# Performance work log

Measured on AMD Instinct MI355X. Metric: run time of the kernel, lower is better.

The kernel has to match this reference:

```python
import jax, jax.numpy as jnp
import numpy as np

N = 50000      # nodes
E = 800000     # edges (before self-loops)
F_IN = 128     # in_dim
H = 8          # heads
C = 16         # out_dim per head
NEG_SLOPE = 0.2
EPS = 1e-5


def setup_inputs() -> dict:
    key = jax.random.key(0)
    ks = jax.random.split(key, 8)
    x = jax.random.normal(ks[0], (N, F_IN), dtype=jnp.float32)
    edge_index = jax.random.randint(ks[1], (2, E), 0, N, dtype=jnp.int64)
    # GAT linear weight (xavier-ish scale), stored as [F_IN, H*C]
    W_gat = jax.random.normal(ks[2], (F_IN, H * C), dtype=jnp.float32) * 0.1
    att_src = jax.random.normal(ks[3], (H, C), dtype=jnp.float32) * 0.1
    att_dst = jax.random.normal(ks[4], (H, C), dtype=jnp.float32) * 0.1
    bias_gat = jnp.zeros((H * C,), dtype=jnp.float32)
    W_skip = jax.random.normal(ks[5], (F_IN, H * C), dtype=jnp.float32) * 0.1
    gamma = jnp.ones((H * C,), dtype=jnp.float32)
    beta = jnp.zeros((H * C,), dtype=jnp.float32)
    return {"x": x, "edge_index": edge_index, "W_gat": W_gat,
            "att_src": att_src, "att_dst": att_dst, "bias_gat": bias_gat,
            "W_skip": W_skip, "gamma": gamma, "beta": beta}


def reference(x, edge_index, W_gat, att_src, att_dst, bias_gat, W_skip, gamma, beta):
    # PyG GATConv default: add self-loops
    loop = jnp.arange(N, dtype=edge_index.dtype)
    src = jnp.concatenate([edge_index[0], loop])  # [E+N]
    dst = jnp.concatenate([edge_index[1], loop])  # [E+N]

    h = (x @ W_gat).reshape(N, H, C)              # [N,H,C]
    a_src = jnp.sum(h * att_src, axis=-1)          # [N,H]
    a_dst = jnp.sum(h * att_dst, axis=-1)          # [N,H]

    e = jax.nn.leaky_relu(a_src[src] + a_dst[dst], NEG_SLOPE)   # [E+N,H]
    # segment softmax over destination nodes
    e_max = jax.ops.segment_max(e, dst, num_segments=N)         # [N,H]
    e_exp = jnp.exp(e - e_max[dst])
    denom = jax.ops.segment_sum(e_exp, dst, num_segments=N)     # [N,H]
    alpha = e_exp / denom[dst]                                   # [E+N,H]

    msg = alpha[:, :, None] * h[src]                             # [E+N,H,C]
    gat_out = jax.ops.segment_sum(msg, dst, num_segments=N)     # [N,H,C]
    gat_out = gat_out.reshape(N, H * C) + bias_gat

    skip_out = x @ W_skip                                        # [N,H*C]
    z = gat_out + 0.1 * skip_out

    mu = jnp.mean(z, axis=-1, keepdims=True)
    var = jnp.mean((z - mu) ** 2, axis=-1, keepdims=True)
    z = (z - mu) * jax.lax.rsqrt(var + EPS) * gamma + beta
    return jax.nn.elu(z)  # dropout is identity in eval mode
```

## Files before the change

kernel.cpp:

```cpp
#include <hip/hip_runtime.h>
#include <hip/hip_bf16.h>

#define N_NODES 50000
#define N_EDGES 800000
#define F_IN    128
#define HC      128
#define NR      8
#define RSZ     6250
#define NCH     16
#define CHSZ    50000

typedef __attribute__((ext_vector_type(8))) short bf16x8;
typedef __attribute__((ext_vector_type(4))) float f32x4;

__device__ __forceinline__ float bf2f(unsigned int u16) {
    return __uint_as_float(u16 << 16);
}
__device__ __forceinline__ unsigned int f2bf(float f) {
    unsigned int u = __float_as_uint(f);
    return (u + 0x7fffu + ((u >> 16) & 1u)) >> 16;
}

__global__ __launch_bounds__(256) void k_hist(
    const int* __restrict__ dst,
    const float* __restrict__ Wg, const float* __restrict__ Ws,
    unsigned short* __restrict__ Bfrag, int* __restrict__ part)
{
    const int bid = blockIdx.x;
    const int tid = threadIdx.x;
    if (bid < 128) {
        __shared__ int hist[RSZ];
        const int r = bid & 7, c = bid >> 3;
        const int nb = r * RSZ;
        for (int i = tid; i < RSZ; i += 256) hist[i] = 0;
        __syncthreads();
        const int4* d4 = (const int4*)(dst + c * CHSZ);
        for (int i = tid; i < CHSZ / 4; i += 256) {
            const int4 v = d4[i];
            int b;
            b = v.x - nb; if ((unsigned)b < (unsigned)RSZ) atomicAdd(&hist[b], 1);
            b = v.y - nb; if ((unsigned)b < (unsigned)RSZ) atomicAdd(&hist[b], 1);
            b = v.z - nb; if ((unsigned)b < (unsigned)RSZ) atomicAdd(&hist[b], 1);
            b = v.w - nb; if ((unsigned)b < (unsigned)RSZ) atomicAdd(&hist[b], 1);
        }
        __syncthreads();
        for (int i = tid; i < RSZ; i += 256)
            part[(size_t)(nb + i) * NCH + c] = hist[i];
    } else {
        const int g = (bid - 128) * 256 + tid;
        if (g < 4096) {
            const int lane = g & 63;
            const int kq = (g >> 6) & 3;
            const int nt = g >> 8;
            const int cc = nt * 16 + (lane & 15);
            const int kbase = kq * 32 + (lane >> 4) * 8;
            const float* Wsel = (cc < 128) ? (Wg + cc) : (Ws + cc - 128);
            unsigned int pk[4];
#pragma unroll
            for (int p = 0; p < 4; p++) {
                const float v0 = Wsel[(size_t)(kbase + 2 * p) * HC];
                const float v1 = Wsel[(size_t)(kbase + 2 * p + 1) * HC];
                pk[p] = f2bf(v0) | (f2bf(v1) << 16);
            }
            *(uint4*)(Bfrag + (size_t)g * 8) = make_uint4(pk[0], pk[1], pk[2], pk[3]);
        }
    }
}

__global__ __launch_bounds__(256) void k_merge(int* __restrict__ part,
                                               int* __restrict__ counts)
{
    const int n = blockIdx.x * 256 + threadIdx.x;
    if (n >= N_NODES) return;
    int4* p = (int4*)(part + (size_t)n * NCH);
    int4 v0 = p[0], v1 = p[1], v2 = p[2], v3 = p[3];
    int vv[16] = {v0.x, v0.y, v0.z, v0.w, v1.x, v1.y, v1.z, v1.w,
                  v2.x, v2.y, v2.z, v2.w, v3.x, v3.y, v3.z, v3.w};
    int run = 0;
#pragma unroll
    for (int c = 0; c < 16; c++) { const int t = vv[c]; vv[c] = run; run += t; }
    counts[n] = run;
    p[0] = make_int4(vv[0], vv[1], vv[2], vv[3]);
    p[1] = make_int4(vv[4], vv[5], vv[6], vv[7]);
    p[2] = make_int4(vv[8], vv[9], vv[10], vv[11]);
    p[3] = make_int4(vv[12], vv[13], vv[14], vv[15]);
}

__global__ __launch_bounds__(256) void k_scanA(const int* __restrict__ counts,
                                               int* __restrict__ row_start,
                                               int* __restrict__ bsum) {
    __shared__ int s[256];
    const int tid = threadIdx.x;
    const int base = blockIdx.x * 1024 + tid * 4;
    int v[4]; int t = 0;
#pragma unroll
    for (int j = 0; j < 4; j++) {
        int idx = base + j;
        v[j] = (idx < N_NODES) ? (counts[idx] + 1) : 0;
        t += v[j];
    }
    s[tid] = t;
    __syncthreads();
    for (int off = 1; off < 256; off <<= 1) {
        int add = (tid >= off) ? s[tid - off] : 0;
        __syncthreads();
        s[tid] += add;
        __syncthreads();
    }
    int excl = s[tid] - t;
#pragma unroll
    for (int j = 0; j < 4; j++) {
        int idx = base + j;
        if (idx < N_NODES) row_start[idx] = excl;
        excl += v[j];
    }
    if (tid == 255) bsum[blockIdx.x] = s[255];
}

__global__ void k_scanB(int* bsum, int nb) {
    int tid = threadIdx.x;
    int v = (tid < nb) ? bsum[tid] : 0;
    int orig = v;
    for (int off = 1; off < 64; off <<= 1) {
        int y = __shfl_up(v, off);
        if (tid >= off) v += y;
    }
    if (tid < nb) bsum[tid] = v - orig;
}

__global__ void k_scanC(int* __restrict__ row_start, const int* __restrict__ bsum,
                        const int* __restrict__ counts, int* __restrict__ csr) {
    int i = blockIdx.x * 256 + threadIdx.x;
    if (i < N_NODES) {
        int rs = row_start[i] + bsum[i >> 10];
        row_start[i] = rs;
        csr[rs + counts[i]] = i;
    }
}

__global__ __launch_bounds__(256) void k_lf(
    const float* __restrict__ x,
    const unsigned short* __restrict__ Bfrag,
    const float* __restrict__ att_s,
    const float* __restrict__ att_d,
    const float* __restrict__ bias,
    unsigned short* __restrict__ h_bf, unsigned int* __restrict__ z0b,
    float* __restrict__ a_src, float* __restrict__ a_dst,
    const int* __restrict__ src, const int* __restrict__ dst,
    const int* __restrict__ row_start, const int* __restrict__ part,
    int* __restrict__ csr)
{
    __shared__ __align__(16) int smem[RSZ];
    const int bid = blockIdx.x;
    const int tid = threadIdx.x;
    int lin = -1, r = 0, c = 0;
    if (bid < 256) {
        const int g = bid >> 4, pos = bid & 15;
        if (pos < 8) { r = pos; c = g; }
        else lin = g * 8 + (pos - 8);
    } else {
        lin = 128 + (bid - 256);
    }

    if (lin < 0) {
        const int nb = r * RSZ;
        for (int b = tid; b < RSZ; b += 256)
            smem[b] = row_start[nb + b] + part[(size_t)(nb + b) * NCH + c];
        __syncthreads();
        const int4* d4 = (const int4*)(dst + c * CHSZ);
        const int4* s4 = (const int4*)(src + c * CHSZ);
        for (int i = tid; i < CHSZ / 4; i += 256) {
            const int4 dv = d4[i];
            const int4 sv = s4[i];
            int b;
            b = dv.x - nb; if ((unsigned)b < (unsigned)RSZ) csr[atomicAdd(&smem[b], 1)] = sv.x;
            b = dv.y - nb; if ((unsigned)b < (unsigned)RSZ) csr[atomicAdd(&smem[b], 1)] = sv.y;
            b = dv.z - nb; if ((unsigned)b < (unsigned)RSZ) csr[atomicAdd(&smem[b], 1)] = sv.z;
            b = dv.w - nb; if ((unsigned)b < (unsigned)RSZ) csr[atomicAdd(&smem[b], 1)] = sv.w;
        }
        return;
    }

    unsigned short* sA = (unsigned short*)smem;
    const int lane = tid & 63;
    const int w = tid >> 6;
    const int nbase = lin * 64;

#pragma unroll
    for (int it = 0; it < 4; it++) {
        const int p = it * 256 + tid;
        const int node = p >> 4;
        const int kg = p & 15;
        const int gn = nbase + node;
        float v[8];
        if (gn < N_NODES) {
            float4 u0 = *(const float4*)(x + (size_t)gn * F_IN + kg * 8);
            float4 u1 = *(const float4*)(x + (size_t)gn * F_IN + kg * 8 + 4);
            v[0] = u0.x; v[1] = u0.y; v[2] = u0.z; v[3] = u0.w;
            v[4] = u1.x; v[5] = u1.y; v[6] = u1.z; v[7] = u1.w;
        } else {
#pragma unroll
            for (int j = 0; j < 8; j++) v[j] = 0.f;
        }
        const int mt = node >> 4, lm = node & 15;
        const int kq = kg >> 2, quad = kg & 3;
        uint4 pk;
        pk.x = f2bf(v[0]) | (f2bf(v[1]) << 16);
        pk.y = f2bf(v[2]) | (f2bf(v[3]) << 16);
        pk.z = f2bf(v[4]) | (f2bf(v[5]) << 16);
        pk.w = f2bf(v[6]) | (f2bf(v[7]) << 16);
        *(uint4*)(sA + ((size_t)((mt * 4 + kq) * 64 + quad * 16 + lm)) * 8) = pk;
    }
    __syncthreads();

    const bf16x8* Bf = (const bf16x8*)Bfrag;
    f32x4 acc[4][4];
#pragma unroll
    for (int mt = 0; mt < 4; mt++)
#pragma unroll
        for (int nt = 0; nt < 4; nt++)
            acc[mt][nt] = (f32x4){0.f, 0.f, 0.f, 0.f};

#pragma unroll
    for (int kq = 0; kq < 4; kq++) {
        bf16x8 aF[4], bF[4];
#pragma unroll
        for (int nt = 0; nt < 4; nt++)
            bF[nt] = Bf[(size_t)(((w * 4 + nt) * 4 + kq) * 64 + lane)];
#pragma unroll
        for (int mt = 0; mt < 4; mt++)
            aF[mt] = *(const bf16x8*)(sA + ((size_t)((mt * 4 + kq) * 64 + lane)) * 8);
#pragma unroll
        for (int mt = 0; mt < 4; mt++)
#pragma unroll
            for (int nt = 0; nt < 4; nt++)
                acc[mt][nt] = __builtin_amdgcn_mfma_f32_16x16x32_bf16(
                    aF[mt], bF[nt], acc[mt][nt], 0, 0, 0);
    }

    const int row4 = (lane >> 4) * 4;
    const int cl = lane & 15;
#pragma unroll
    for (int mt = 0; mt < 4; mt++) {
#pragma unroll
        for (int nt = 0; nt < 4; nt++) {
            const int cc = w * 64 + nt * 16 + cl;
            f32x4 d = acc[mt][nt];
            if (cc < 128) {
                const float asv = att_s[cc];
                const float adv = att_d[cc];
                float ps[4], pd[4];
#pragma unroll
                for (int rr = 0; rr < 4; rr++) { ps[rr] = d[rr] * asv; pd[rr] = d[rr] * adv; }
#pragma unroll
                for (int m = 1; m <= 8; m <<= 1) {
#pragma unroll
                    for (int rr = 0; rr < 4; rr++) {
                        ps[rr] += __shfl_xor(ps[rr], m);
                        pd[rr] += __shfl_xor(pd[rr], m);
                    }
                }
                const int head = w * 4 + nt;
#pragma unroll
                for (int rr = 0; rr < 4; rr++) {
                    const int gn = nbase + mt * 16 + row4 + rr;
                    if (gn < N_NODES) {
                        h_bf[(size_t)gn * HC + cc] = (unsigned short)f2bf(d[rr]);
                        if (cl == 0) {
                            a_src[gn * 8 + head] = ps[rr];
                            a_dst[gn * 8 + head] = pd[rr];
                        }
                    }
                }
            } else {
                const int cz = cc - 128;
                const float bv = bias[cz];
#pragma unroll
                for (int rr = 0; rr < 4; rr++) {
                    const int gn = nbase + mt * 16 + row4 + rr;
                    const float val = 0.1f * d[rr] + bv;
                    const float oth = __shfl_xor(val, 1);
                    if ((cl & 1) == 0 && gn < N_NODES) {
                        z0b[(size_t)gn * 64 + (cz >> 1)] =
                            f2bf(val) | (f2bf(oth) << 16);
                    }
                }
            }
        }
    }
}

__global__ __launch_bounds__(256) void k_agg(
    const uint2* __restrict__ h2,
    const uint2* __restrict__ z0b,
    const float* __restrict__ a_src, const float* __restrict__ a_dst,
    const int* __restrict__ row_start, const int* __restrict__ counts,
    const int* __restrict__ csr,
    const float* __restrict__ gamma, const float* __restrict__ beta,
    float* __restrict__ out)
{
    const int tid = threadIdx.x;
    const int lane = tid & 63;
    const int l = lane & 31;
    const int n = blockIdx.x * 8 + ((tid >> 6) << 1) + (lane >> 5);
    const int head = l >> 2;

    const float adn = a_dst[n * 8 + head];
    const int rs = row_start[n];
    const int cnt = counts[n] + 1;

    float d_acc = 0.f, a0 = 0.f, a1 = 0.f, a2 = 0.f, a3 = 0.f;
    for (int i = 0; i < cnt; i += 4) {
        int s[4]; float ae[4], mk[4]; uint2 hp[4];
#pragma unroll
        for (int j = 0; j < 4; j++) {
            const int e = i + j;
            const int ec = (e < cnt) ? e : (cnt - 1);
            mk[j] = (e < cnt) ? 1.f : 0.f;
            s[j] = csr[rs + ec];
        }
#pragma unroll
        for (int j = 0; j < 4; j++) ae[j] = a_src[s[j] * 8 + head];
#pragma unroll
        for (int j = 0; j < 4; j++) hp[j] = h2[(size_t)s[j] * 32 + l];
#pragma unroll
        for (int j = 0; j < 4; j++) {
            float e = ae[j] + adn;
            e = (e > 0.f) ? e : 0.2f * e;
            const float wgt = __expf(e) * mk[j];
            d_acc += wgt;
            a0 += wgt * bf2f(hp[j].x & 0xffffu);
            a1 += wgt * bf2f(hp[j].x >> 16);
            a2 += wgt * bf2f(hp[j].y & 0xffffu);
            a3 += wgt * bf2f(hp[j].y >> 16);
        }
    }
    const float inv = 1.0f / d_acc;
    const uint2 zp = z0b[(size_t)n * 32 + l];
    float y0 = a0 * inv + bf2f(zp.x & 0xffffu);
    float y1 = a1 * inv + bf2f(zp.x >> 16);
    float y2 = a2 * inv + bf2f(zp.y & 0xffffu);
    float y3 = a3 * inv + bf2f(zp.y >> 16);

    float ss = y0 + y1 + y2 + y3;
#pragma unroll
    for (int off = 1; off < 32; off <<= 1) ss += __shfl_xor(ss, off);
    const float mu = ss * (1.0f / 128.0f);
    const float d0 = y0 - mu, d1 = y1 - mu, d2 = y2 - mu, d3 = y3 - mu;
    float vs = d0 * d0 + d1 * d1 + d2 * d2 + d3 * d3;
#pragma unroll
    for (int off = 1; off < 32; off <<= 1) vs += __shfl_xor(vs, off);
    const float rstd = rsqrtf(vs * (1.0f / 128.0f) + 1e-5f);

    const float4 gv = *(const float4*)(gamma + l * 4);
    const float4 bv = *(const float4*)(beta + l * 4);
    float o0 = d0 * rstd * gv.x + bv.x;
    float o1 = d1 * rstd * gv.y + bv.y;
    float o2 = d2 * rstd * gv.z + bv.z;
    float o3 = d3 * rstd * gv.w + bv.w;
    o0 = (o0 > 0.f) ? o0 : (__expf(o0) - 1.0f);
    o1 = (o1 > 0.f) ? o1 : (__expf(o1) - 1.0f);
    o2 = (o2 > 0.f) ? o2 : (__expf(o2) - 1.0f);
    o3 = (o3 > 0.f) ? o3 : (__expf(o3) - 1.0f);

    *(float4*)(out + (size_t)n * HC + l * 4) = make_float4(o0, o1, o2, o3);
}

extern "C" void kernel_launch(void* const* d_in, const int* in_sizes, int n_in,
                              void* d_out, int out_size, void* d_ws, size_t ws_size,
                              hipStream_t stream) {
    const float* x   = (const float*)d_in[0];
    const int*   ei  = (const int*)d_in[1];
    const float* Wg  = (const float*)d_in[2];
    const float* as_ = (const float*)d_in[3];
    const float* ad_ = (const float*)d_in[4];
    const float* bg  = (const float*)d_in[5];
    const float* Wsk = (const float*)d_in[6];
    const float* gm  = (const float*)d_in[7];
    const float* bt  = (const float*)d_in[8];
    float* out = (float*)d_out;

    char* wsb = (char*)d_ws;
    unsigned short* h_bf  = (unsigned short*)wsb;
    unsigned int*   z0b   = (unsigned int*)(wsb + 12800000);
    float*          a_src = (float*)(wsb + 25600000);
    float*          a_dst = (float*)(wsb + 27200000);
    unsigned short* Bfrag = (unsigned short*)(wsb + 28800000);
    int*   counts = (int*)(wsb + 28865536);
    int*   row_st = (int*)(wsb + 29065728);
    int*   bsum   = (int*)(wsb + 29265920);
    int*   csr    = (int*)(wsb + 29266944);
    int*   part   = (int*)(wsb + 32666944);

    const int* src = ei;
    const int* dst = ei + N_EDGES;

    k_hist <<<144, 256, 0, stream>>>(dst, Wg, Wsk, Bfrag, part);
    k_merge<<<196, 256, 0, stream>>>(part, counts);
    k_scanA<<<49, 256, 0, stream>>>(counts, row_st, bsum);
    k_scanB<<<1, 64, 0, stream>>>(bsum, 49);
    k_scanC<<<196, 256, 0, stream>>>(row_st, bsum, counts, csr);
    k_lf   <<<910, 256, 0, stream>>>(x, Bfrag, as_, ad_, bg, h_bf, z0b,
                                     a_src, a_dst, src, dst, row_st, part, csr);
    k_agg  <<<N_NODES / 8, 256, 0, stream>>>((const uint2*)h_bf, (const uint2*)z0b,
                                             a_src, a_dst, row_st, counts, csr,
                                             gm, bt, out);
}
```

Measured before the change: 213.2 us.

## Split histogram/scatter into more node ranges, fold merge into scan, widen agg unroll

Doubles the number of destination-node ranges (16 ranges of 3125), so the histogram and CSR-scatter phases run on 256 blocks instead of 128, each with a smaller shared-memory table. The per-node prefix merge kernel is folded into the first scan kernel, which removes one launch and one pass over the partial counts. The scatter blocks in the fused linear kernel are interleaved one in four with the GEMM blocks. The aggregation loop now gathers 8 edges per iteration instead of 4, giving more loads in flight at the cost of more registers. In exchange, every block still rereads each 50000-edge chunk of the destination (and, in the scatter, source) arrays, so twice as many blocks means twice as much of that redundant reading.

```diff
diff --git a/kernel.cpp b/kernel.cpp
--- a/kernel.cpp
+++ b/kernel.cpp
@@ -5,8 +5,8 @@
 #define N_EDGES 800000
 #define F_IN    128
 #define HC      128
-#define NR      8
-#define RSZ     6250
+#define NR      16
+#define RSZ     3125
 #define NCH     16
 #define CHSZ    50000
 
@@ -28,9 +28,9 @@
 {
     const int bid = blockIdx.x;
     const int tid = threadIdx.x;
-    if (bid < 128) {
+    if (bid < 256) {
         __shared__ int hist[RSZ];
-        const int r = bid & 7, c = bid >> 3;
+        const int r = bid & 15, c = bid >> 4;
         const int nb = r * RSZ;
         for (int i = tid; i < RSZ; i += 256) hist[i] = 0;
         __syncthreads();
@@ -47,7 +47,7 @@
         for (int i = tid; i < RSZ; i += 256)
             part[(size_t)(nb + i) * NCH + c] = hist[i];
     } else {
-        const int g = (bid - 128) * 256 + tid;
+        const int g = (bid - 256) * 256 + tid;
         if (g < 4096) {
             const int lane = g & 63;
             const int kq = (g >> 6) & 3;
@@ -67,36 +67,32 @@
     }
 }
 
-__global__ __launch_bounds__(256) void k_merge(int* __restrict__ part,
-                                               int* __restrict__ counts)
+__global__ __launch_bounds__(256) void k_scanA(
+    int* __restrict__ part, int* __restrict__ counts,
+    int* __restrict__ row_start, int* __restrict__ bsum)
 {
-    const int n = blockIdx.x * 256 + threadIdx.x;
-    if (n >= N_NODES) return;
-    int4* p = (int4*)(part + (size_t)n * NCH);
-    int4 v0 = p[0], v1 = p[1], v2 = p[2], v3 = p[3];
-    int vv[16] = {v0.x, v0.y, v0.z, v0.w, v1.x, v1.y, v1.z, v1.w,
-                  v2.x, v2.y, v2.z, v2.w, v3.x, v3.y, v3.z, v3.w};
-    int run = 0;
-#pragma unroll
-    for (int c = 0; c < 16; c++) { const int t = vv[c]; vv[c] = run; run += t; }
-    counts[n] = run;
-    p[0] = make_int4(vv[0], vv[1], vv[2], vv[3]);
-    p[1] = make_int4(vv[4], vv[5], vv[6], vv[7]);
-    p[2] = make_int4(vv[8], vv[9], vv[10], vv[11]);
-    p[3] = make_int4(vv[12], vv[13], vv[14], vv[15]);
-}
-
-__global__ __launch_bounds__(256) void k_scanA(const int* __restrict__ counts,
-                                               int* __restrict__ row_start,
-                                               int* __restrict__ bsum) {
     __shared__ int s[256];
     const int tid = threadIdx.x;
     const int base = blockIdx.x * 1024 + tid * 4;
     int v[4]; int t = 0;
 #pragma unroll
     for (int j = 0; j < 4; j++) {
-        int idx = base + j;
-        v[j] = (idx < N_NODES) ? (counts[idx] + 1) : 0;
+        const int idx = base + j;
+        if (idx < N_NODES) {
+            int4* p = (int4*)(part + (size_t)idx * NCH);
+            int4 a0 = p[0], a1 = p[1], a2 = p[2], a3 = p[3];
+            int vv[16] = {a0.x, a0.y, a0.z, a0.w, a1.x, a1.y, a1.z, a1.w,
+                          a2.x, a2.y, a2.z, a2.w, a3.x, a3.y, a3.z, a3.w};
+            int run = 0;
+#pragma unroll
+            for (int c = 0; c < 16; c++) { const int q = vv[c]; vv[c] = run; run += q; }
+            p[0] = make_int4(vv[0], vv[1], vv[2], vv[3]);
+            p[1] = make_int4(vv[4], vv[5], vv[6], vv[7]);
+            p[2] = make_int4(vv[8], vv[9], vv[10], vv[11]);
+            p[3] = make_int4(vv[12], vv[13], vv[14], vv[15]);
+            counts[idx] = run;
+            v[j] = run + 1;
+        } else v[j] = 0;
         t += v[j];
     }
     s[tid] = t;
@@ -110,7 +106,7 @@
     int excl = s[tid] - t;
 #pragma unroll
     for (int j = 0; j < 4; j++) {
-        int idx = base + j;
+        const int idx = base + j;
         if (idx < N_NODES) row_start[idx] = excl;
         excl += v[j];
     }
@@ -150,35 +146,34 @@
     const int* __restrict__ row_start, const int* __restrict__ part,
     int* __restrict__ csr)
 {
-    __shared__ __align__(16) int smem[RSZ];
+    __shared__ __align__(16) int smem[4096];
     const int bid = blockIdx.x;
     const int tid = threadIdx.x;
-    int lin = -1, r = 0, c = 0;
-    if (bid < 256) {
-        const int g = bid >> 4, pos = bid & 15;
-        if (pos < 8) { r = pos; c = g; }
-        else lin = g * 8 + (pos - 8);
+    int lin;
+    if (bid < 1024) {
+        if ((bid & 3) == 0) {
+            const int f = bid >> 2;
+            const int r = f & 15, c = f >> 4;
+            const int nb = r * RSZ;
+            for (int b = tid; b < RSZ; b += 256)
+                smem[b] = row_start[nb + b] + part[(size_t)(nb + b) * NCH + c];
+            __syncthreads();
+            const int4* d4 = (const int4*)(dst + c * CHSZ);
+            const int4* s4 = (const int4*)(src + c * CHSZ);
+            for (int i = tid; i < CHSZ / 4; i += 256) {
+                const int4 dv = d4[i];
+                const int4 sv = s4[i];
+                int b;
+                b = dv.x - nb; if ((unsigned)b < (unsigned)RSZ) csr[atomicAdd(&smem[b], 1)] = sv.x;
+                b = dv.y - nb; if ((unsigned)b < (unsigned)RSZ) csr[atomicAdd(&smem[b], 1)] = sv.y;
+                b = dv.z - nb; if ((unsigned)b < (unsigned)RSZ) csr[atomicAdd(&smem[b], 1)] = sv.z;
+                b = dv.w - nb; if ((unsigned)b < (unsigned)RSZ) csr[atomicAdd(&smem[b], 1)] = sv.w;
+            }
+            return;
+        }
+        lin = bid - (bid >> 2) - 1;
     } else {
-        lin = 128 + (bid - 256);
-    }
-
-    if (lin < 0) {
-        const int nb = r * RSZ;
-        for (int b = tid; b < RSZ; b += 256)
-            smem[b] = row_start[nb + b] + part[(size_t)(nb + b) * NCH + c];
-        __syncthreads();
-        const int4* d4 = (const int4*)(dst + c * CHSZ);
-        const int4* s4 = (const int4*)(src + c * CHSZ);
-        for (int i = tid; i < CHSZ / 4; i += 256) {
-            const int4 dv = d4[i];
-            const int4 sv = s4[i];
-            int b;
-            b = dv.x - nb; if ((unsigned)b < (unsigned)RSZ) csr[atomicAdd(&smem[b], 1)] = sv.x;
-            b = dv.y - nb; if ((unsigned)b < (unsigned)RSZ) csr[atomicAdd(&smem[b], 1)] = sv.y;
-            b = dv.z - nb; if ((unsigned)b < (unsigned)RSZ) csr[atomicAdd(&smem[b], 1)] = sv.z;
-            b = dv.w - nb; if ((unsigned)b < (unsigned)RSZ) csr[atomicAdd(&smem[b], 1)] = sv.w;
-        }
-        return;
+        lin = bid - 256;
     }
 
     unsigned short* sA = (unsigned short*)smem;
@@ -310,21 +305,21 @@
     const int cnt = counts[n] + 1;
 
     float d_acc = 0.f, a0 = 0.f, a1 = 0.f, a2 = 0.f, a3 = 0.f;
-    for (int i = 0; i < cnt; i += 4) {
-        int s[4]; float ae[4], mk[4]; uint2 hp[4];
-#pragma unroll
-        for (int j = 0; j < 4; j++) {
+    for (int i = 0; i < cnt; i += 8) {
+        int s[8]; float ae[8], mk[8]; uint2 hp[8];
+#pragma unroll
+        for (int j = 0; j < 8; j++) {
             const int e = i + j;
             const int ec = (e < cnt) ? e : (cnt - 1);
             mk[j] = (e < cnt) ? 1.f : 0.f;
             s[j] = csr[rs + ec];
         }
 #pragma unroll
-        for (int j = 0; j < 4; j++) ae[j] = a_src[s[j] * 8 + head];
-#pragma unroll
-        for (int j = 0; j < 4; j++) hp[j] = h2[(size_t)s[j] * 32 + l];
-#pragma unroll
-        for (int j = 0; j < 4; j++) {
+        for (int j = 0; j < 8; j++) ae[j] = a_src[s[j] * 8 + head];
+#pragma unroll
+        for (int j = 0; j < 8; j++) hp[j] = h2[(size_t)s[j] * 32 + l];
+#pragma unroll
+        for (int j = 0; j < 8; j++) {
             float e = ae[j] + adn;
             e = (e > 0.f) ? e : 0.2f * e;
             const float wgt = __expf(e) * mk[j];
@@ -395,13 +390,12 @@
     const int* src = ei;
     const int* dst = ei + N_EDGES;
 
-    k_hist <<<144, 256, 0, stream>>>(dst, Wg, Wsk, Bfrag, part);
-    k_merge<<<196, 256, 0, stream>>>(part, counts);
-    k_scanA<<<49, 256, 0, stream>>>(counts, row_st, bsum);
+    k_hist <<<272, 256, 0, stream>>>(dst, Wg, Wsk, Bfrag, part);
+    k_scanA<<<49, 256, 0, stream>>>(part, counts, row_st, bsum);
     k_scanB<<<1, 64, 0, stream>>>(bsum, 49);
     k_scanC<<<196, 256, 0, stream>>>(row_st, bsum, counts, csr);
-    k_lf   <<<910, 256, 0, stream>>>(x, Bfrag, as_, ad_, bg, h_bf, z0b,
-                                     a_src, a_dst, src, dst, row_st, part, csr);
+    k_lf   <<<1038, 256, 0, stream>>>(x, Bfrag, as_, ad_, bg, h_bf, z0b,
+                                      a_src, a_dst, src, dst, row_st, part, csr);
     k_agg  <<<N_NODES / 8, 256, 0, stream>>>((const uint2*)h_bf, (const uint2*)z0b,
                                              a_src, a_dst, row_st, counts, csr,
                                              gm, bt, out);
```

Result: slower. 252.7 us (+18.6%).
